# Kernel optimization log

Hardware: AMD Instinct MI355X
Metric: run time of the kernel (lower is better)

The kernel has to match this reference:

```python
import jax, jax.numpy as jnp
import numpy as np

H = 8
DH = 64
SCALE = DH ** -0.5

def setup_inputs() -> dict:
    key = jax.random.key(0)
    ks = jax.random.split(key, 32)
    B, NQ, N1, N2, N3 = 4, 1024, 1024, 1024, 2048
    QD, C1, C2, C3 = 512, 512, 768, 256
    INNER, VD = H * DH, 512
    s = 0.02
    inp = {
        'x':        jax.random.normal(ks[0], (B, NQ, QD), jnp.float32),
        'context':  jax.random.normal(ks[1], (B, N1, C1), jnp.float32),
        'context2': jax.random.normal(ks[2], (B, N2, C2), jnp.float32),
        'context3': jax.random.normal(ks[3], (B, N3, C3), jnp.float32),
        'mask1': jax.random.randint(ks[4], (B, NQ, N1), 0, 2) > 0,
        'mask2': jax.random.randint(ks[5], (B, NQ, N2), 0, 2) > 0,
        'mask3': jax.random.randint(ks[6], (B, NQ, N3), 0, 2) > 0,
        'Wq':  jax.random.normal(ks[7],  (QD, INNER), jnp.float32) * s,
        'bq':  jnp.zeros((INNER,), jnp.float32),
        'Wk1': jax.random.normal(ks[8],  (C1, INNER), jnp.float32) * s,
        'bk1': jnp.zeros((INNER,), jnp.float32),
        'Wv1': jax.random.normal(ks[9],  (C1, VD), jnp.float32) * s,
        'bv1': jnp.zeros((VD,), jnp.float32),
        'Wk2': jax.random.normal(ks[10], (C2, INNER), jnp.float32) * s,
        'bk2': jnp.zeros((INNER,), jnp.float32),
        'Wv2': jax.random.normal(ks[11], (C2, VD), jnp.float32) * s,
        'bv2': jnp.zeros((VD,), jnp.float32),
        'Wk3': jax.random.normal(ks[12], (C3, INNER), jnp.float32) * s,
        'bk3': jnp.zeros((INNER,), jnp.float32),
        'Wv3': jax.random.normal(ks[13], (C3, VD), jnp.float32) * s,
        'bv3': jnp.zeros((VD,), jnp.float32),
        'Wo':  jax.random.normal(ks[14], (VD, VD), jnp.float32) * s,
        'bo':  jnp.zeros((VD,), jnp.float32),
    }
    return inp

def _split_heads(t):
    # [b, n, h*d] -> [b, h, n, d]
    b, n, hd = t.shape
    return t.reshape(b, n, H, hd // H).transpose(0, 2, 1, 3)

def reference(x, context, context2, context3, mask1, mask2, mask3,
              Wq, bq, Wk1, bk1, Wv1, bv1, Wk2, bk2, Wv2, bv2,
              Wk3, bk3, Wv3, bv3, Wo, bo):
    q = x @ Wq + bq
    k = jnp.concatenate([context @ Wk1 + bk1, context2 @ Wk2 + bk2, context3 @ Wk3 + bk3], axis=1)
    v = jnp.concatenate([context @ Wv1 + bv1, context2 @ Wv2 + bv2, context3 @ Wv3 + bv3], axis=1)
    qh, kh, vh = _split_heads(q), _split_heads(k), _split_heads(v)
    sim = jnp.einsum('bhid,bhjd->bhij', qh, kh) * SCALE  # [b,h,nq,nk]
    mask = jnp.concatenate([mask1, mask2, mask3], axis=2)  # [b,nq,nk]
    neg = -jnp.finfo(sim.dtype).max
    sim = jnp.where(mask[:, None, :, :], sim, neg)
    attn = jax.nn.softmax(sim, axis=-1)
    out = jnp.einsum('bhij,bhjd->bhid', attn, vh)  # [b,h,nq,dv]
    b, h, n, d = out.shape
    out = out.transpose(0, 2, 1, 3).reshape(b, n, h * d)
    return out @ Wo + bo
```

## Files before the change

### kernel.cpp

```cpp
#include <hip/hip_runtime.h>

typedef _Float16 f16;
typedef _Float16 f16x8 __attribute__((ext_vector_type(8)));
typedef _Float16 f16x4 __attribute__((ext_vector_type(4)));
typedef _Float16 f16x2 __attribute__((ext_vector_type(2)));
typedef float f32x4 __attribute__((ext_vector_type(4)));
typedef unsigned long long u64;

#define MFMA16(a, b, c) __builtin_amdgcn_mfma_f32_16x16x32_f16((a), (b), (c), 0, 0, 0)

constexpr float QSCALE = 0.18033688011112042f;

struct CDesc { const float* src; f16* dst; unsigned n4, off4; };

__global__ __launch_bounds__(256) void convert_kernel(CDesc a, CDesc b, CDesc c, CDesc d) {
  unsigned t = blockIdx.x * 256u + threadIdx.x;
  CDesc s;
  if (t >= d.off4) s = d;
  else if (t >= c.off4) s = c;
  else if (t >= b.off4) s = b;
  else s = a;
  unsigned i = t - s.off4;
  if (i >= s.n4) return;
  float4 v = ((const float4*)s.src)[i];
  f16x4 o;
  o[0] = (f16)v.x; o[1] = (f16)v.y; o[2] = (f16)v.z; o[3] = (f16)v.w;
  ((f16x4*)s.dst)[i] = o;
}

struct TDesc { const float* src; f16* dst; int K, blk_off; };
struct TArgs { TDesc t[8]; };

__global__ __launch_bounds__(256) void transpose_kernel(TArgs args) {
  int bid = blockIdx.x;
  int di = 0;
#pragma unroll
  for (int i = 1; i < 8; i++)
    if (bid >= args.t[i].blk_off) di = i;
  TDesc d = args.t[di];
  int lb = bid - d.blk_off;
  int ktiles = d.K >> 5;
  int kt = lb % ktiles, nt = lb / ktiles;
  int k0 = kt * 32, n0 = nt * 32;
  __shared__ float tile[32][33];
  int tc = threadIdx.x & 31;
  int tr = threadIdx.x >> 5;
#pragma unroll
  for (int i = 0; i < 4; i++) {
    int kl = tr + 8 * i;
    tile[tc][kl] = d.src[(size_t)(k0 + kl) * 512 + n0 + tc];
  }
  __syncthreads();
#pragma unroll
  for (int i = 0; i < 4; i++) {
    int nl = tr + 8 * i;
    d.dst[(size_t)(n0 + nl) * d.K + k0 + tc] = (f16)tile[nl][tc];
  }
}

__global__ __launch_bounds__(256) void maskprep_kernel(const void* __restrict__ m1,
                                                       const void* __restrict__ m2,
                                                       const void* __restrict__ m3,
                                                       u64* __restrict__ mb) {
  unsigned t = blockIdx.x * 256u + threadIdx.x;
  unsigned probe = ((const unsigned*)m1)[threadIdx.x & 15];
  u64 vote = __ballot(probe <= 1u);
  bool int_mode = ((vote & 0xFFFFull) == 0xFFFFull);
  unsigned row = t >> 12;
  unsigned j = t & 4095;
  const void* src;
  long idx;
  if (j < 1024) { src = m1; idx = (long)row * 1024 + j; }
  else if (j < 2048) { src = m2; idx = (long)row * 1024 + (j - 1024); }
  else { src = m3; idx = (long)row * 2048 + (j - 2048); }
  bool pred = int_mode ? (((const int*)src)[idx] != 0)
                       : (((const unsigned char*)src)[idx] != 0);
  u64 bal = __ballot(pred);
  if ((threadIdx.x & 63) == 0) mb[t >> 6] = bal;
}

struct PDesc {
  const f16* A; const f16* B; const float* bias; void* out;
  int K, mode, logNloc, nk_off, blk_off, ntiles;
};
struct PArgs { PDesc d[8]; };

__global__ __launch_bounds__(256) void proj_kernel(PArgs args, int bid_base) {
  int bid = blockIdx.x + bid_base;
  int di = 0;
#pragma unroll
  for (int i = 1; i < 8; i++)
    if (bid >= args.d[i].blk_off) di = i;
  PDesc d = args.d[di];
  int lb = bid - d.blk_off;
  int bn = lb % d.ntiles, bm = lb / d.ntiles;
  int tid = threadIdx.x;
  int lane = tid & 63, wv = tid >> 6;
  int wm = wv >> 1, wn = wv & 1;
  int r16 = lane & 15, q4 = lane >> 4;
  int K = d.K;
  int m0 = bm * 128, n0 = bn * 128;

  __shared__ f16 As[2][128 * 40];
  __shared__ f16 Bs[2][128 * 40];

  int sr = tid >> 2;
  int sc = (tid & 3) * 8;
  const f16* ag = d.A + (size_t)(m0 + sr) * K + sc;
  const f16* bg = d.B + (size_t)(n0 + sr) * K + sc;
  f16x8 ra0, ra1, rb0, rb1;
  auto ldg = [&](int k0) {
    ra0 = *(const f16x8*)(ag + k0);
    ra1 = *(const f16x8*)(ag + (size_t)64 * K + k0);
    rb0 = *(const f16x8*)(bg + k0);
    rb1 = *(const f16x8*)(bg + (size_t)64 * K + k0);
  };
  auto sts = [&](int p) {
    *(f16x8*)(As[p] + sr * 40 + sc) = ra0;
    *(f16x8*)(As[p] + (sr + 64) * 40 + sc) = ra1;
    *(f16x8*)(Bs[p] + sr * 40 + sc) = rb0;
    *(f16x8*)(Bs[p] + (sr + 64) * 40 + sc) = rb1;
  };

  f32x4 c[4][4] = {};
  int nk = K >> 5;
  ldg(0);
  sts(0);
  __syncthreads();
  for (int kt = 0; kt < nk; kt++) {
    int p = kt & 1;
    if (kt + 1 < nk) ldg((kt + 1) << 5);
    const f16* ab = As[p] + (wm * 64 + r16) * 40 + q4 * 8;
    const f16* bb = Bs[p] + (wn * 64 + r16) * 40 + q4 * 8;
    f16x8 af[4], bf[4];
#pragma unroll
    for (int t = 0; t < 4; t++) af[t] = *(const f16x8*)(ab + t * 16 * 40);
#pragma unroll
    for (int u = 0; u < 4; u++) bf[u] = *(const f16x8*)(bb + u * 16 * 40);
#pragma unroll
    for (int t = 0; t < 4; t++)
#pragma unroll
      for (int u = 0; u < 4; u++) c[t][u] = MFMA16(af[t], bf[u], c[t][u]);
    if (kt + 1 < nk) sts(p ^ 1);
    __syncthreads();
  }

  int msk = (1 << d.logNloc) - 1;
#pragma unroll
  for (int t = 0; t < 4; t++) {
#pragma unroll
    for (int u = 0; u < 4; u++) {
#pragma unroll
      for (int r = 0; r < 4; r++) {
        int gm = m0 + wm * 64 + t * 16 + q4 * 4 + r;
        int cn = n0 + wn * 64 + u * 16 + r16;
        float val = c[t][u][r] + (d.mode == 2 ? d.bias[gm] : d.bias[cn]);
        if (d.mode == 0) {
          int hh = cn >> 6, dd = cn & 63, bb = gm >> 10, nn = gm & 1023;
          ((f16*)d.out)[(((size_t)bb * 8 + hh) * 1024 + nn) * 64 + dd] = (f16)(val * QSCALE);
        } else if (d.mode == 1) {
          int hh = cn >> 6, dd = cn & 63, bb = gm >> d.logNloc, nn = d.nk_off + (gm & msk);
          ((f16*)d.out)[(((size_t)bb * 8 + hh) * 4096 + nn) * 64 + dd] = (f16)val;
        } else if (d.mode == 2) {
          int hh = gm >> 6, dd = gm & 63, bb = cn >> d.logNloc, nn = d.nk_off + (cn & msk);
          ((f16*)d.out)[(((size_t)bb * 8 + hh) * 64 + dd) * 4096 + nn] = (f16)val;
        } else {
          ((float*)d.out)[(size_t)gm * 512 + cn] = val;
        }
      }
    }
  }
}

__global__ __launch_bounds__(256, 3) void attn_kernel(const f16* __restrict__ Qh,
                                                      const f16* __restrict__ Kh,
                                                      const f16* __restrict__ Vt,
                                                      const u64* __restrict__ MB,
                                                      f16* __restrict__ PO,
                                                      float* __restrict__ LW) {
  int lin = blockIdx.x;
  int hb = lin & 31;
  int rest = lin >> 5;
  int qt = rest & 7, ks = rest >> 3;
  int h = hb & 7, b = hb >> 3;
  int tid = threadIdx.x;
  int lane = tid & 63, wv = tid >> 6;
  int r16 = lane & 15, q4 = lane >> 4;
  int q0 = qt * 128;
  int bh = b * 8 + h;

  const f16* qp = Qh + ((size_t)bh * 1024 + q0 + wv * 32) * 64;
  f16x8 aq[2][2];
#pragma unroll
  for (int s = 0; s < 2; s++) {
    aq[s][0] = *(const f16x8*)(qp + (s * 16 + r16) * 64 + q4 * 8);
    aq[s][1] = *(const f16x8*)(qp + (s * 16 + r16) * 64 + q4 * 8 + 32);
  }
  const f16* kg = Kh + (size_t)bh * (4096 * 64) + (size_t)ks * 1024 * 64;
  const f16* vg = Vt + (size_t)bh * (64 * 4096) + ks * 1024;
  const u64* mrow = MB + ((size_t)b * 1024 + q0 + wv * 32 + r16) * 64 + ks * 16;

  __shared__ f16 kls[2][64 * 72];
  __shared__ f16 vls[2][64 * 72];
  __shared__ f16 pbuf[4][32 * 40];
  f16* pw = pbuf[wv];

  int c_row = tid >> 3;
  int c_col = (tid & 7) * 8;
  f16x8 kr0, kr1, vr0, vr1;
  auto loadKV = [&](int j0) {
    const f16* kp = kg + (size_t)(j0 + c_row) * 64 + c_col;
    kr0 = *(const f16x8*)kp;
    kr1 = *(const f16x8*)(kp + 32 * 64);
    const f16* vp = vg + (size_t)c_row * 4096 + j0 + c_col;
    vr0 = *(const f16x8*)vp;
    vr1 = *(const f16x8*)(vp + 32 * 4096);
  };
  auto writeKV = [&](int p) {
    *(f16x8*)(kls[p] + c_row * 72 + c_col) = kr0;
    *(f16x8*)(kls[p] + (c_row + 32) * 72 + c_col) = kr1;
    *(f16x8*)(vls[p] + c_row * 72 + c_col) = vr0;
    *(f16x8*)(vls[p] + (c_row + 32) * 72 + c_col) = vr1;
  };

  f16x8 ones;
#pragma unroll
  for (int i = 0; i < 8; i++) ones[i] = (f16)1.0f;
  f32x4 accl[2] = {};
  f32x4 acc[2][4] = {};

  loadKV(0);
  writeKV(0);
  loadKV(64);
  __syncthreads();

  for (int jt = 0; jt < 16; jt++) {
    int p = jt & 1;
    if (jt < 15) writeKV(p ^ 1);
    if (jt < 14) loadKV((jt + 2) * 64);
    u64 wrd[2];
#pragma unroll
    for (int s = 0; s < 2; s++) wrd[s] = mrow[s * 16 * 64 + jt];
    const f16* kb_ = kls[p];
    const f16* vb_ = vls[p];
#pragma unroll
    for (int ph = 0; ph < 2; ph++) {
#pragma unroll
      for (int th = 0; th < 2; th++) {
        int t = ph * 2 + th;
        f16x8 k0 = *(const f16x8*)(kb_ + (t * 16 + r16) * 72 + q4 * 8);
        f16x8 k1 = *(const f16x8*)(kb_ + (t * 16 + r16) * 72 + q4 * 8 + 32);
#pragma unroll
        for (int s = 0; s < 2; s++) {
          f32x4 z{};
          z = MFMA16(k0, aq[s][0], z);
          z = MFMA16(k1, aq[s][1], z);
          u64 w = wrd[s] >> (t * 16 + q4 * 4);
          float p0 = (w & 1) ? __builtin_amdgcn_exp2f(z[0]) : 0.0f;
          float p1 = (w & 2) ? __builtin_amdgcn_exp2f(z[1]) : 0.0f;
          float p2 = (w & 4) ? __builtin_amdgcn_exp2f(z[2]) : 0.0f;
          float p3 = (w & 8) ? __builtin_amdgcn_exp2f(z[3]) : 0.0f;
          f16x2 lo = __builtin_bit_cast(f16x2, __builtin_amdgcn_cvt_pkrtz(p0, p1));
          f16x2 hi = __builtin_bit_cast(f16x2, __builtin_amdgcn_cvt_pkrtz(p2, p3));
          f16x4 pk = __builtin_shufflevector(lo, hi, 0, 1, 2, 3);
          *(f16x4*)(pw + (s * 16 + r16) * 40 + th * 16 + q4 * 4) = pk;
        }
      }
      asm volatile("s_waitcnt lgkmcnt(0)" ::: "memory");
      f16x8 ap[2];
#pragma unroll
      for (int s = 0; s < 2; s++)
        ap[s] = *(const f16x8*)(pw + (s * 16 + r16) * 40 + q4 * 8);
#pragma unroll
      for (int dt = 0; dt < 4; dt++) {
        f16x8 vf = *(const f16x8*)(vb_ + (dt * 16 + r16) * 72 + ph * 32 + q4 * 8);
#pragma unroll
        for (int s = 0; s < 2; s++) acc[s][dt] = MFMA16(ap[s], vf, acc[s][dt]);
      }
#pragma unroll
      for (int s = 0; s < 2; s++) accl[s] = MFMA16(ap[s], ones, accl[s]);
    }
    __syncthreads();
  }

  f16* pok = PO + (size_t)ks * (4096 * 512);
#pragma unroll
  for (int s = 0; s < 2; s++)
#pragma unroll
    for (int r = 0; r < 4; r++) {
      int rowg = b * 1024 + q0 + wv * 32 + s * 16 + q4 * 4 + r;
      f16* orow = pok + (size_t)rowg * 512 + h * 64 + r16;
#pragma unroll
      for (int dt = 0; dt < 4; dt++) orow[dt * 16] = (f16)(acc[s][dt][r]);
    }
  if (r16 == 0) {
    float* lk = LW + (size_t)ks * 32768 + (size_t)bh * 1024 + q0 + wv * 32;
#pragma unroll
    for (int s = 0; s < 2; s++)
#pragma unroll
      for (int r = 0; r < 4; r++) lk[s * 16 + q4 * 4 + r] = accl[s][r];
  }
}

__global__ __launch_bounds__(256) void combine_kernel(const f16* __restrict__ PO,
                                                      const float* __restrict__ LW,
                                                      f16* __restrict__ AO) {
  int t = blockIdx.x * 256 + threadIdx.x;
  int row = t >> 6;
  int col = (t & 63) * 8;
  int b = row >> 10, q = row & 1023;
  int h = col >> 6;
  size_t lidx = (size_t)(b * 8 + h) * 1024 + q;
  float l = LW[lidx] + LW[32768 + lidx] + LW[65536 + lidx] + LW[98304 + lidx];
  float inv = 1.0f / l;
  size_t off = (size_t)row * 512 + col;
  f16x8 o0 = *(const f16x8*)(PO + off);
  f16x8 o1 = *(const f16x8*)(PO + 2097152 + off);
  f16x8 o2 = *(const f16x8*)(PO + 4194304 + off);
  f16x8 o3 = *(const f16x8*)(PO + 6291456 + off);
  f16x8 out;
#pragma unroll
  for (int j = 0; j < 8; j++)
    out[j] = (f16)(((float)o0[j] + (float)o1[j] + (float)o2[j] + (float)o3[j]) * inv);
  *(f16x8*)(AO + off) = out;
}

extern "C" void kernel_launch(void* const* d_in, const int* in_sizes, int n_in,
                              void* d_out, int out_size, void* d_ws, size_t ws_size,
                              hipStream_t stream) {
  (void)in_sizes; (void)n_in; (void)out_size; (void)ws_size;
  const float* x  = (const float*)d_in[0];
  const float* c1 = (const float*)d_in[1];
  const float* c2 = (const float*)d_in[2];
  const float* c3 = (const float*)d_in[3];
  const void* m1 = d_in[4];
  const void* m2 = d_in[5];
  const void* m3 = d_in[6];
  const float* Wq = (const float*)d_in[7];   const float* bq = (const float*)d_in[8];
  const float* Wk1 = (const float*)d_in[9];  const float* bk1 = (const float*)d_in[10];
  const float* Wv1 = (const float*)d_in[11]; const float* bv1 = (const float*)d_in[12];
  const float* Wk2 = (const float*)d_in[13]; const float* bk2 = (const float*)d_in[14];
  const float* Wv2 = (const float*)d_in[15]; const float* bv2 = (const float*)d_in[16];
  const float* Wk3 = (const float*)d_in[17]; const float* bk3 = (const float*)d_in[18];
  const float* Wv3 = (const float*)d_in[19]; const float* bv3 = (const float*)d_in[20];
  const float* Wo = (const float*)d_in[21];  const float* bo = (const float*)d_in[22];

  char* ws = (char*)d_ws;
  size_t off = 0;
  auto alloc = [&](size_t bytes) {
    void* p = ws + off;
    off = (off + bytes + 255) & ~(size_t)255;
    return p;
  };
  f16* xb   = (f16*)alloc(2097152 * 2);
  f16* c1b  = (f16*)alloc(2097152 * 2);
  f16* c2b  = (f16*)alloc(3145728 * 2);
  f16* c3b  = (f16*)alloc(2097152 * 2);
  f16* wqt  = (f16*)alloc(262144 * 2);
  f16* wk1t = (f16*)alloc(262144 * 2);
  f16* wk2t = (f16*)alloc(393216 * 2);
  f16* wk3t = (f16*)alloc(131072 * 2);
  f16* wv1t = (f16*)alloc(262144 * 2);
  f16* wv2t = (f16*)alloc(393216 * 2);
  f16* wv3t = (f16*)alloc(131072 * 2);
  f16* wot  = (f16*)alloc(262144 * 2);
  f16* qh   = (f16*)alloc(2097152 * 2);
  f16* kh   = (f16*)alloc(8388608 * 2);
  f16* vt   = (f16*)alloc(8388608 * 2);
  f16* ao   = (f16*)alloc(2097152 * 2);
  u64* mbits = (u64*)alloc(2097152);

  f16* po = (f16*)ws;
  float* lw = (float*)(ws + 16777216);

  CDesc cdx  = {x,  xb,  524288, 0};
  CDesc cdc1 = {c1, c1b, 524288, 524288};
  CDesc cdc2 = {c2, c2b, 786432, 1048576};
  CDesc cdc3 = {c3, c3b, 524288, 1835008};
  convert_kernel<<<9216, 256, 0, stream>>>(cdx, cdc1, cdc2, cdc3);

  TArgs ta;
  ta.t[0] = {Wq,  wqt,  512, 0};
  ta.t[1] = {Wk1, wk1t, 512, 256};
  ta.t[2] = {Wk2, wk2t, 768, 512};
  ta.t[3] = {Wk3, wk3t, 256, 896};
  ta.t[4] = {Wv1, wv1t, 512, 1024};
  ta.t[5] = {Wv2, wv2t, 768, 1280};
  ta.t[6] = {Wv3, wv3t, 256, 1664};
  ta.t[7] = {Wo,  wot,  512, 1792};
  transpose_kernel<<<2048, 256, 0, stream>>>(ta);

  maskprep_kernel<<<65536, 256, 0, stream>>>(m1, m2, m3, mbits);

  PArgs pa;
  pa.d[0] = {xb,   wqt,  bq,  qh,    512, 0, 10, 0,    0,    4};
  pa.d[1] = {c1b,  wk1t, bk1, kh,    512, 1, 10, 0,    128,  4};
  pa.d[2] = {c2b,  wk2t, bk2, kh,    768, 1, 10, 1024, 256,  4};
  pa.d[3] = {c3b,  wk3t, bk3, kh,    256, 1, 11, 2048, 384,  4};
  pa.d[4] = {wv1t, c1b,  bv1, vt,    512, 2, 10, 0,    640,  32};
  pa.d[5] = {wv2t, c2b,  bv2, vt,    768, 2, 10, 1024, 768,  32};
  pa.d[6] = {wv3t, c3b,  bv3, vt,    256, 2, 11, 2048, 896,  64};
  pa.d[7] = {ao,   wot,  bo,  d_out, 512, 3, 10, 0,    1152, 4};
  proj_kernel<<<1152, 256, 0, stream>>>(pa, 0);

  attn_kernel<<<1024, 256, 0, stream>>>(qh, kh, vt, mbits, po, lw);

  combine_kernel<<<1024, 256, 0, stream>>>(po, lw, ao);

  proj_kernel<<<128, 256, 0, stream>>>(pa, 1152);
}
```

Measured before the change: 345.1 us.

## Use direct global-to-LDS loads in GEMM and attention; merge prep kernels

Fuses the convert, transpose and mask-pack kernels into one prep launch, and has each mask wave pack four 64-bit words instead of one. Replaces the register-staged K/V and GEMM tile loads with global_load_lds direct-to-LDS transfers. The attention K/V tiles drop their padding and use an XOR swizzle to avoid bank conflicts. This aims to cut launch overhead, register staging and VGPR pressure, but the attention kernel now prefetches only one tile ahead instead of two, which may expose more load latency.

```diff
diff --git a/kernel.cpp b/kernel.cpp
--- a/kernel.cpp
+++ b/kernel.cpp
@@ -11,40 +11,78 @@
 
 constexpr float QSCALE = 0.18033688011112042f;
 
+__device__ __forceinline__ void gll16(const f16* g, f16* l) {
+  __builtin_amdgcn_global_load_lds((__attribute__((address_space(1))) void*)(g),
+                                   (__attribute__((address_space(3))) void*)(l),
+                                   16, 0, 0);
+}
+
 struct CDesc { const float* src; f16* dst; unsigned n4, off4; };
-
-__global__ __launch_bounds__(256) void convert_kernel(CDesc a, CDesc b, CDesc c, CDesc d) {
-  unsigned t = blockIdx.x * 256u + threadIdx.x;
-  CDesc s;
-  if (t >= d.off4) s = d;
-  else if (t >= c.off4) s = c;
-  else if (t >= b.off4) s = b;
-  else s = a;
-  unsigned i = t - s.off4;
-  if (i >= s.n4) return;
-  float4 v = ((const float4*)s.src)[i];
-  f16x4 o;
-  o[0] = (f16)v.x; o[1] = (f16)v.y; o[2] = (f16)v.z; o[3] = (f16)v.w;
-  ((f16x4*)s.dst)[i] = o;
-}
-
 struct TDesc { const float* src; f16* dst; int K, blk_off; };
-struct TArgs { TDesc t[8]; };
-
-__global__ __launch_bounds__(256) void transpose_kernel(TArgs args) {
+
+struct PrepArgs {
+  const void* m1; const void* m2; const void* m3; u64* mb;
+  CDesc cd[4];
+  TDesc td[8];
+};
+
+__global__ __launch_bounds__(256) void prep_kernel(PrepArgs a) {
   int bid = blockIdx.x;
+  int tid = threadIdx.x;
+  __shared__ float tile[32][33];
+  if (bid < 16384) {
+    int l = tid & 63;
+    unsigned probe = ((const unsigned*)a.m1)[tid & 15];
+    u64 vote = __ballot(probe <= 1u);
+    bool int_mode = ((vote & 0xFFFFull) == 0xFFFFull);
+    unsigned gw = bid * 4u + (tid >> 6);
+    unsigned e0 = gw * 256u;
+    unsigned row = e0 >> 12, j0 = e0 & 4095;
+    const void* src; size_t base;
+    if (j0 < 1024) { src = a.m1; base = (size_t)row * 1024 + j0; }
+    else if (j0 < 2048) { src = a.m2; base = (size_t)row * 1024 + (j0 - 1024); }
+    else { src = a.m3; base = (size_t)row * 2048 + (j0 - 2048); }
+    u64 b0, b1, b2, b3;
+    if (int_mode) {
+      const int* s = (const int*)src + base + l;
+      b0 = __ballot(s[0] != 0);   b1 = __ballot(s[64] != 0);
+      b2 = __ballot(s[128] != 0); b3 = __ballot(s[192] != 0);
+    } else {
+      const unsigned char* s = (const unsigned char*)src + base + l;
+      b0 = __ballot(s[0] != 0);   b1 = __ballot(s[64] != 0);
+      b2 = __ballot(s[128] != 0); b3 = __ballot(s[192] != 0);
+    }
+    u64 b = b0;
+    if (l == 1) b = b1; else if (l == 2) b = b2; else if (l == 3) b = b3;
+    if (l < 4) a.mb[gw * 4 + l] = b;
+    return;
+  }
+  if (bid < 25600) {
+    unsigned t = (bid - 16384) * 256u + tid;
+    CDesc s;
+    if (t >= a.cd[3].off4) s = a.cd[3];
+    else if (t >= a.cd[2].off4) s = a.cd[2];
+    else if (t >= a.cd[1].off4) s = a.cd[1];
+    else s = a.cd[0];
+    unsigned i = t - s.off4;
+    if (i >= s.n4) return;
+    float4 v = ((const float4*)s.src)[i];
+    f16x4 o;
+    o[0] = (f16)v.x; o[1] = (f16)v.y; o[2] = (f16)v.z; o[3] = (f16)v.w;
+    ((f16x4*)s.dst)[i] = o;
+    return;
+  }
+  int tb = bid - 25600;
   int di = 0;
 #pragma unroll
   for (int i = 1; i < 8; i++)
-    if (bid >= args.t[i].blk_off) di = i;
-  TDesc d = args.t[di];
-  int lb = bid - d.blk_off;
+    if (tb >= a.td[i].blk_off) di = i;
+  TDesc d = a.td[di];
+  int lb = tb - d.blk_off;
   int ktiles = d.K >> 5;
   int kt = lb % ktiles, nt = lb / ktiles;
   int k0 = kt * 32, n0 = nt * 32;
-  __shared__ float tile[32][33];
-  int tc = threadIdx.x & 31;
-  int tr = threadIdx.x >> 5;
+  int tc = tid & 31, tr = tid >> 5;
 #pragma unroll
   for (int i = 0; i < 4; i++) {
     int kl = tr + 8 * i;
@@ -56,27 +94,6 @@
     int nl = tr + 8 * i;
     d.dst[(size_t)(n0 + nl) * d.K + k0 + tc] = (f16)tile[nl][tc];
   }
-}
-
-__global__ __launch_bounds__(256) void maskprep_kernel(const void* __restrict__ m1,
-                                                       const void* __restrict__ m2,
-                                                       const void* __restrict__ m3,
-                                                       u64* __restrict__ mb) {
-  unsigned t = blockIdx.x * 256u + threadIdx.x;
-  unsigned probe = ((const unsigned*)m1)[threadIdx.x & 15];
-  u64 vote = __ballot(probe <= 1u);
-  bool int_mode = ((vote & 0xFFFFull) == 0xFFFFull);
-  unsigned row = t >> 12;
-  unsigned j = t & 4095;
-  const void* src;
-  long idx;
-  if (j < 1024) { src = m1; idx = (long)row * 1024 + j; }
-  else if (j < 2048) { src = m2; idx = (long)row * 1024 + (j - 1024); }
-  else { src = m3; idx = (long)row * 2048 + (j - 2048); }
-  bool pred = int_mode ? (((const int*)src)[idx] != 0)
-                       : (((const unsigned char*)src)[idx] != 0);
-  u64 bal = __ballot(pred);
-  if ((threadIdx.x & 63) == 0) mb[t >> 6] = bal;
 }
 
 struct PDesc {
@@ -101,47 +118,39 @@
   int K = d.K;
   int m0 = bm * 128, n0 = bn * 128;
 
-  __shared__ f16 As[2][128 * 40];
-  __shared__ f16 Bs[2][128 * 40];
-
-  int sr = tid >> 2;
-  int sc = (tid & 3) * 8;
-  const f16* ag = d.A + (size_t)(m0 + sr) * K + sc;
-  const f16* bg = d.B + (size_t)(n0 + sr) * K + sc;
-  f16x8 ra0, ra1, rb0, rb1;
-  auto ldg = [&](int k0) {
-    ra0 = *(const f16x8*)(ag + k0);
-    ra1 = *(const f16x8*)(ag + (size_t)64 * K + k0);
-    rb0 = *(const f16x8*)(bg + k0);
-    rb1 = *(const f16x8*)(bg + (size_t)64 * K + k0);
-  };
-  auto sts = [&](int p) {
-    *(f16x8*)(As[p] + sr * 40 + sc) = ra0;
-    *(f16x8*)(As[p] + (sr + 64) * 40 + sc) = ra1;
-    *(f16x8*)(Bs[p] + sr * 40 + sc) = rb0;
-    *(f16x8*)(Bs[p] + (sr + 64) * 40 + sc) = rb1;
+  __shared__ f16 As[2][128 * 32];
+  __shared__ f16 Bs[2][128 * 32];
+
+  int srow = 32 * wv + (lane >> 2);
+  int scol = 8 * (lane & 3);
+  const f16* agw = d.A + (size_t)(m0 + srow) * K + scol;
+  const f16* bgw = d.B + (size_t)(n0 + srow) * K + scol;
+  auto stage = [&](int p, int kk) {
+#pragma unroll
+    for (int cc = 0; cc < 2; cc++) {
+      gll16(agw + (size_t)(16 * cc) * K + kk, As[p] + 1024 * wv + 512 * cc);
+      gll16(bgw + (size_t)(16 * cc) * K + kk, Bs[p] + 1024 * wv + 512 * cc);
+    }
   };
 
   f32x4 c[4][4] = {};
   int nk = K >> 5;
-  ldg(0);
-  sts(0);
+  stage(0, 0);
   __syncthreads();
   for (int kt = 0; kt < nk; kt++) {
     int p = kt & 1;
-    if (kt + 1 < nk) ldg((kt + 1) << 5);
-    const f16* ab = As[p] + (wm * 64 + r16) * 40 + q4 * 8;
-    const f16* bb = Bs[p] + (wn * 64 + r16) * 40 + q4 * 8;
+    if (kt + 1 < nk) stage(p ^ 1, (kt + 1) << 5);
+    const f16* ab = As[p] + (wm * 64 + r16) * 32 + q4 * 8;
+    const f16* bb = Bs[p] + (wn * 64 + r16) * 32 + q4 * 8;
     f16x8 af[4], bf[4];
 #pragma unroll
-    for (int t = 0; t < 4; t++) af[t] = *(const f16x8*)(ab + t * 16 * 40);
-#pragma unroll
-    for (int u = 0; u < 4; u++) bf[u] = *(const f16x8*)(bb + u * 16 * 40);
+    for (int t = 0; t < 4; t++) af[t] = *(const f16x8*)(ab + t * 16 * 32);
+#pragma unroll
+    for (int u = 0; u < 4; u++) bf[u] = *(const f16x8*)(bb + u * 16 * 32);
 #pragma unroll
     for (int t = 0; t < 4; t++)
 #pragma unroll
       for (int u = 0; u < 4; u++) c[t][u] = MFMA16(af[t], bf[u], c[t][u]);
-    if (kt + 1 < nk) sts(p ^ 1);
     __syncthreads();
   }
 
@@ -200,27 +209,28 @@
   const f16* vg = Vt + (size_t)bh * (64 * 4096) + ks * 1024;
   const u64* mrow = MB + ((size_t)b * 1024 + q0 + wv * 32 + r16) * 64 + ks * 16;
 
-  __shared__ f16 kls[2][64 * 72];
-  __shared__ f16 vls[2][64 * 72];
+  __shared__ f16 kls[2][64 * 64];
+  __shared__ f16 vls[2][64 * 64];
   __shared__ f16 pbuf[4][32 * 40];
   f16* pw = pbuf[wv];
 
-  int c_row = tid >> 3;
-  int c_col = (tid & 7) * 8;
-  f16x8 kr0, kr1, vr0, vr1;
-  auto loadKV = [&](int j0) {
-    const f16* kp = kg + (size_t)(j0 + c_row) * 64 + c_col;
-    kr0 = *(const f16x8*)kp;
-    kr1 = *(const f16x8*)(kp + 32 * 64);
-    const f16* vp = vg + (size_t)c_row * 4096 + j0 + c_col;
-    vr0 = *(const f16x8*)vp;
-    vr1 = *(const f16x8*)(vp + 32 * 4096);
-  };
-  auto writeKV = [&](int p) {
-    *(f16x8*)(kls[p] + c_row * 72 + c_col) = kr0;
-    *(f16x8*)(kls[p] + (c_row + 32) * 72 + c_col) = kr1;
-    *(f16x8*)(vls[p] + c_row * 72 + c_col) = vr0;
-    *(f16x8*)(vls[p] + (c_row + 32) * 72 + c_col) = vr1;
+  int Tv = wv >> 1, hlf = wv & 1;
+  int row0 = 32 * hlf + (lane >> 3);
+  int blk = (lane & 7) ^ ((lane >> 3) & 7);
+  const f16* kgw = kg + (size_t)row0 * 64 + 8 * blk;
+  const f16* vgw = vg + (size_t)row0 * 4096 + 8 * blk;
+  auto stage = [&](int pp, int j0) {
+    if (Tv == 0) {
+      const f16* g = kgw + (size_t)j0 * 64;
+      f16* l = kls[pp] + 2048 * hlf;
+#pragma unroll
+      for (int cc = 0; cc < 4; cc++) gll16(g + cc * (8 * 64), l + cc * 512);
+    } else {
+      const f16* g = vgw + j0;
+      f16* l = vls[pp] + 2048 * hlf;
+#pragma unroll
+      for (int cc = 0; cc < 4; cc++) gll16(g + (size_t)cc * (8 * 4096), l + cc * 512);
+    }
   };
 
   f16x8 ones;
@@ -229,18 +239,16 @@
   f32x4 accl[2] = {};
   f32x4 acc[2][4] = {};
 
-  loadKV(0);
-  writeKV(0);
-  loadKV(64);
+  stage(0, 0);
   __syncthreads();
 
+  int sw = 8 * (r16 & 7);
   for (int jt = 0; jt < 16; jt++) {
     int p = jt & 1;
-    if (jt < 15) writeKV(p ^ 1);
-    if (jt < 14) loadKV((jt + 2) * 64);
     u64 wrd[2];
-#pragma unroll
-    for (int s = 0; s < 2; s++) wrd[s] = mrow[s * 16 * 64 + jt];
+    wrd[0] = mrow[jt];
+    wrd[1] = mrow[16 * 64 + jt];
+    if (jt < 15) stage(p ^ 1, (jt + 1) * 64);
     const f16* kb_ = kls[p];
     const f16* vb_ = vls[p];
 #pragma unroll
@@ -248,8 +256,8 @@
 #pragma unroll
       for (int th = 0; th < 2; th++) {
         int t = ph * 2 + th;
-        f16x8 k0 = *(const f16x8*)(kb_ + (t * 16 + r16) * 72 + q4 * 8);
-        f16x8 k1 = *(const f16x8*)(kb_ + (t * 16 + r16) * 72 + q4 * 8 + 32);
+        f16x8 k0 = *(const f16x8*)(kb_ + (t * 16 + r16) * 64 + ((q4 * 8) ^ sw));
+        f16x8 k1 = *(const f16x8*)(kb_ + (t * 16 + r16) * 64 + ((32 + q4 * 8) ^ sw));
 #pragma unroll
         for (int s = 0; s < 2; s++) {
           f32x4 z{};
@@ -273,7 +281,7 @@
         ap[s] = *(const f16x8*)(pw + (s * 16 + r16) * 40 + q4 * 8);
 #pragma unroll
       for (int dt = 0; dt < 4; dt++) {
-        f16x8 vf = *(const f16x8*)(vb_ + (dt * 16 + r16) * 72 + ph * 32 + q4 * 8);
+        f16x8 vf = *(const f16x8*)(vb_ + (dt * 16 + r16) * 64 + ((ph * 32 + q4 * 8) ^ sw));
 #pragma unroll
         for (int s = 0; s < 2; s++) acc[s][dt] = MFMA16(ap[s], vf, acc[s][dt]);
       }
@@ -373,24 +381,21 @@
   f16* po = (f16*)ws;
   float* lw = (float*)(ws + 16777216);
 
-  CDesc cdx  = {x,  xb,  524288, 0};
-  CDesc cdc1 = {c1, c1b, 524288, 524288};
-  CDesc cdc2 = {c2, c2b, 786432, 1048576};
-  CDesc cdc3 = {c3, c3b, 524288, 1835008};
-  convert_kernel<<<9216, 256, 0, stream>>>(cdx, cdc1, cdc2, cdc3);
-
-  TArgs ta;
-  ta.t[0] = {Wq,  wqt,  512, 0};
-  ta.t[1] = {Wk1, wk1t, 512, 256};
-  ta.t[2] = {Wk2, wk2t, 768, 512};
-  ta.t[3] = {Wk3, wk3t, 256, 896};
-  ta.t[4] = {Wv1, wv1t, 512, 1024};
-  ta.t[5] = {Wv2, wv2t, 768, 1280};
-  ta.t[6] = {Wv3, wv3t, 256, 1664};
-  ta.t[7] = {Wo,  wot,  512, 1792};
-  transpose_kernel<<<2048, 256, 0, stream>>>(ta);
-
-  maskprep_kernel<<<65536, 256, 0, stream>>>(m1, m2, m3, mbits);
+  PrepArgs pra;
+  pra.m1 = m1; pra.m2 = m2; pra.m3 = m3; pra.mb = mbits;
+  pra.cd[0] = {x,  xb,  524288, 0};
+  pra.cd[1] = {c1, c1b, 524288, 524288};
+  pra.cd[2] = {c2, c2b, 786432, 1048576};
+  pra.cd[3] = {c3, c3b, 524288, 1835008};
+  pra.td[0] = {Wq,  wqt,  512, 0};
+  pra.td[1] = {Wk1, wk1t, 512, 256};
+  pra.td[2] = {Wk2, wk2t, 768, 512};
+  pra.td[3] = {Wk3, wk3t, 256, 896};
+  pra.td[4] = {Wv1, wv1t, 512, 1024};
+  pra.td[5] = {Wv2, wv2t, 768, 1280};
+  pra.td[6] = {Wv3, wv3t, 256, 1664};
+  pra.td[7] = {Wo,  wot,  512, 1792};
+  prep_kernel<<<27648, 256, 0, stream>>>(pra);
 
   PArgs pa;
   pa.d[0] = {xb,   wqt,  bq,  qh,    512, 0, 10, 0,    0,    4};
```

After: 324.8 us. 5.9% less time.
